# Kernel optimization log

Measured on AMD Instinct MI355X. Metric: run time of the kernel, lower is better.

Reference implementation:

```python
import jax, jax.numpy as jnp
import numpy as np

N, NFEAT, NHID, NCLASS, NLAYERS = 8192, 512, 128, 40, 3
NEG = -9e15

def _sparse_adj(key, n, density=0.002):
    u = jax.random.uniform(key, (n, n), dtype=jnp.float32)
    return jnp.where(u < density, u / density, 0.0)

def setup_inputs() -> dict:
    key = jax.random.key(0)
    ks = jax.random.split(key, 12)
    return {
        "x": jax.random.normal(ks[0], (N, NFEAT), dtype=jnp.float32),
        "adj1": _sparse_adj(ks[1], N),
        "adj2": _sparse_adj(ks[2], N),
        "adj_att": _sparse_adj(ks[3], N),
        "fc1_w": jax.random.normal(ks[4], (NLAYERS, NHID, NFEAT), dtype=jnp.float32) * (1.0 / np.sqrt(NFEAT)),
        "fc1_b": jnp.zeros((NLAYERS, NHID), jnp.float32),
        "Q_w": jax.random.normal(ks[5], (NLAYERS - 1, NHID, NHID), dtype=jnp.float32) * (1.0 / np.sqrt(NHID)),
        "Q_b": jnp.zeros((NLAYERS - 1, NHID), jnp.float32),
        "K_w": jax.random.normal(ks[6], (NLAYERS - 1, NHID, NHID), dtype=jnp.float32) * (1.0 / np.sqrt(NHID)),
        "K_b": jnp.zeros((NLAYERS - 1, NHID), jnp.float32),
        "hop_select": jnp.ones((NLAYERS,), jnp.float32),
        "w": jnp.ones((NLAYERS - 1, 2), jnp.float32),
        "clf_w": jax.random.normal(ks[7], (NCLASS, NHID * NLAYERS), dtype=jnp.float32) * (1.0 / np.sqrt(NHID * NLAYERS)),
        "clf_b": jnp.zeros((NCLASS,), jnp.float32),
    }

def _l2_normalize(x, eps=1e-12):
    # F.normalize(x, p=2, dim=1)
    n = jnp.sqrt(jnp.sum(x * x, axis=1, keepdims=True))
    return x / jnp.maximum(n, eps)

def reference(x, adj1, adj2, adj_att, fc1_w, fc1_b, Q_w, Q_b, K_w, K_b,
              hop_select, w, clf_w, clf_b):
    adj_list = [None, adj1, adj2]
    mask = jax.nn.softmax(hop_select)  # hop selection weights, shape [nlayers]
    outs = []
    for i in range(NLAYERS):
        tmp = x @ fc1_w[i].T + fc1_b[i]  # [N, nhid]
        if adj_list[i] is not None:
            adj = adj_list[i]
            W_att = jax.nn.softmax(w[i - 1])  # [2]
            tmp_att = adj_att @ tmp           # [N, nhid]
            # GCN1: linear then propagate with adj_att (act='None')
            Q = adj_att @ (tmp_att @ Q_w[i - 1].T + Q_b[i - 1])
            K = adj_att @ (tmp_att @ K_w[i - 1].T + K_b[i - 1])
            scores = Q @ K.T                  # [N, N]
            scores = jnp.where(adj > 0, scores, NEG)
            attention = jax.nn.softmax(scores, axis=-1) * W_att[0] + adj * W_att[1]
            tmp = attention @ tmp             # [N, nhid]
        tmp = _l2_normalize(tmp)
        outs.append(mask[i] * tmp)
    final = jnp.concatenate(outs, axis=1)     # [N, nhid*nlayers]
    out = jax.nn.relu(final) @ clf_w.T + clf_b  # dropout is identity in eval
    return jax.nn.log_softmax(out, axis=1)
```

## Files before the change

kernel.cpp:

```cpp
#include <hip/hip_runtime.h>
#include <hip/hip_bf16.h>

#define NN     8192
#define NF4    2048
#define NFEAT  512
#define NHID   128
#define NCLASS 40
#define NLAY   3
#define CAPA   128
#define FSZ    ((size_t)NN * NHID)

typedef float f32x4 __attribute__((ext_vector_type(4)));

__global__ void k_setup(const float* __restrict__ hop, const float* __restrict__ w,
                        float* __restrict__ mask, float* __restrict__ watt,
                        float* __restrict__ colsum) {
    int t = threadIdx.x;
    colsum[t] = 0.f;
    if (t == 0) {
        float m = fmaxf(fmaxf(hop[0], hop[1]), hop[2]);
        float e0 = expf(hop[0] - m), e1 = expf(hop[1] - m), e2 = expf(hop[2] - m);
        float s = e0 + e1 + e2;
        mask[0] = e0 / s; mask[1] = e1 / s; mask[2] = e2 / s;
        for (int l = 0; l < 2; ++l) {
            float a = w[2 * l], b = w[2 * l + 1];
            float mm = fmaxf(a, b);
            float ea = expf(a - mm), eb = expf(b - mm);
            float ss = ea + eb;
            watt[2 * l] = ea / ss; watt[2 * l + 1] = eb / ss;
        }
    }
}

__global__ __launch_bounds__(256) void k_gemm_fc1(
    const float* __restrict__ A, const float* __restrict__ B,
    const float* __restrict__ bias, float* __restrict__ C)
{
    __shared__ float As[32][132];
    __shared__ float Bs[32][132];
    const int tid = threadIdx.x, tx = tid & 15, ty = tid >> 4;
    const int bm = blockIdx.x * 128, bn = blockIdx.y * 128;
    float acc[8][8] = {};

    for (int kt = 0; kt < NFEAT; kt += 32) {
        #pragma unroll
        for (int it = 0; it < 4; ++it) {
            int L = tid + it * 256;
            int r = L >> 3, c4 = (L & 7) * 4;
            f32x4 va = *reinterpret_cast<const f32x4*>(&A[(size_t)(bm + r) * NFEAT + kt + c4]);
            As[c4 + 0][r] = va[0]; As[c4 + 1][r] = va[1]; As[c4 + 2][r] = va[2]; As[c4 + 3][r] = va[3];
            f32x4 vb = *reinterpret_cast<const f32x4*>(&B[(size_t)(bn + r) * NFEAT + kt + c4]);
            Bs[c4 + 0][r] = vb[0]; Bs[c4 + 1][r] = vb[1]; Bs[c4 + 2][r] = vb[2]; Bs[c4 + 3][r] = vb[3];
        }
        __syncthreads();
        #pragma unroll
        for (int kk = 0; kk < 32; ++kk) {
            f32x4 ra0 = *reinterpret_cast<const f32x4*>(&As[kk][ty * 8]);
            f32x4 ra1 = *reinterpret_cast<const f32x4*>(&As[kk][ty * 8 + 4]);
            f32x4 rb0 = *reinterpret_cast<const f32x4*>(&Bs[kk][tx * 8]);
            f32x4 rb1 = *reinterpret_cast<const f32x4*>(&Bs[kk][tx * 8 + 4]);
            float ra[8] = {ra0[0], ra0[1], ra0[2], ra0[3], ra1[0], ra1[1], ra1[2], ra1[3]};
            float rb[8] = {rb0[0], rb0[1], rb0[2], rb0[3], rb1[0], rb1[1], rb1[2], rb1[3]};
            #pragma unroll
            for (int i = 0; i < 8; ++i)
                #pragma unroll
                for (int j = 0; j < 8; ++j)
                    acc[i][j] = fmaf(ra[i], rb[j], acc[i][j]);
        }
        __syncthreads();
    }
    #pragma unroll
    for (int i = 0; i < 8; ++i) {
        int m = bm + ty * 8 + i;
        #pragma unroll
        for (int j = 0; j < 8; ++j) {
            int n = bn + tx * 8 + j;
            C[(size_t)(n >> 7) * FSZ + (size_t)m * NHID + (n & 127)] = acc[i][j] + bias[n];
        }
    }
}

__global__ __launch_bounds__(256) void k_gemm_qkm(
    const float* __restrict__ T2, const float* __restrict__ Qw, const float* __restrict__ Kw,
    const float* __restrict__ Qb, const float* __restrict__ Kb,
    const float* __restrict__ rowsumA, float* __restrict__ QKm)
{
    __shared__ float As[64][68];
    __shared__ float Bs[64][68];
    const int tid = threadIdx.x, tx = tid & 15, ty = tid >> 4;
    const int bm = blockIdx.x * 64, bn = blockIdx.y * 64, Lz = blockIdx.z;
    const float* A = T2 + (size_t)Lz * FSZ;
    const float* Bp; const float* bp; int bc;
    if (bn < 128) { Bp = Qw + (size_t)Lz * NHID * NHID; bp = Qb + (size_t)Lz * NHID; bc = bn; }
    else          { Bp = Kw + (size_t)Lz * NHID * NHID; bp = Kb + (size_t)Lz * NHID; bc = bn - 128; }
    float* C = QKm + (size_t)Lz * NN * 256;
    float acc[4][4] = {};

    for (int kt = 0; kt < NHID; kt += 64) {
        #pragma unroll
        for (int it = 0; it < 4; ++it) {
            int L = tid + it * 256;
            int r = L >> 4, c4 = (L & 15) * 4;
            f32x4 va = *reinterpret_cast<const f32x4*>(&A[(size_t)(bm + r) * NHID + kt + c4]);
            As[c4 + 0][r] = va[0]; As[c4 + 1][r] = va[1]; As[c4 + 2][r] = va[2]; As[c4 + 3][r] = va[3];
            f32x4 vb = *reinterpret_cast<const f32x4*>(&Bp[(size_t)(bc + r) * NHID + kt + c4]);
            Bs[c4 + 0][r] = vb[0]; Bs[c4 + 1][r] = vb[1]; Bs[c4 + 2][r] = vb[2]; Bs[c4 + 3][r] = vb[3];
        }
        __syncthreads();
        #pragma unroll
        for (int kk = 0; kk < 64; ++kk) {
            f32x4 ra4 = *reinterpret_cast<const f32x4*>(&As[kk][ty * 4]);
            f32x4 rb4 = *reinterpret_cast<const f32x4*>(&Bs[kk][tx * 4]);
            #pragma unroll
            for (int i = 0; i < 4; ++i)
                #pragma unroll
                for (int j = 0; j < 4; ++j)
                    acc[i][j] = fmaf(ra4[i], rb4[j], acc[i][j]);
        }
        __syncthreads();
    }
    #pragma unroll
    for (int i = 0; i < 4; ++i) {
        int m = bm + ty * 4 + i;
        float rs = rowsumA[m];
        #pragma unroll
        for (int j = 0; j < 4; ++j) {
            int n = bn + tx * 4 + j;
            C[(size_t)m * 256 + n] = acc[i][j] + rs * bp[bc + tx * 4 + j];
        }
    }
}

__global__ __launch_bounds__(256) void k_extract(
    const float* __restrict__ adj, int* __restrict__ cnt,
    int* __restrict__ cols, float* __restrict__ vals, float* __restrict__ rowsum)
{
    int row = blockIdx.x, t = threadIdx.x;
    __shared__ int lcnt;
    __shared__ float lsum;
    if (t == 0) { lcnt = 0; lsum = 0.f; }
    __syncthreads();
    const f32x4* arow = reinterpret_cast<const f32x4*>(adj + (size_t)row * NN);
    int* rc = cols + (size_t)row * CAPA;
    float* rv = vals + (size_t)row * CAPA;
    for (int c4 = t; c4 < NF4; c4 += 256) {
        f32x4 v = __builtin_nontemporal_load(&arow[c4]);
        #pragma unroll
        for (int k = 0; k < 4; ++k) {
            if (v[k] > 0.f) {
                int p = atomicAdd(&lcnt, 1);
                atomicAdd(&lsum, v[k]);
                if (p < CAPA) { rc[p] = c4 * 4 + k; rv[p] = v[k]; }
            }
        }
    }
    __syncthreads();
    if (t == 0) { cnt[row] = lcnt < CAPA ? lcnt : CAPA; rowsum[row] = lsum; }
}

__global__ __launch_bounds__(256) void k_prep(
    const float* __restrict__ tmps, const float* __restrict__ mask,
    float* __restrict__ outsb, float* __restrict__ colsum)
{
    int b = blockIdx.x, t = threadIdx.x;
    __shared__ float ws[4];
    if (b < NN / 2) {
        int row = b * 2 + (t >> 7), tt = t & 127;
        float v = tmps[(size_t)row * NHID + tt];
        float s = v * v;
        #pragma unroll
        for (int m = 32; m; m >>= 1) s += __shfl_xor(s, m);
        if ((t & 63) == 0) ws[t >> 6] = s;
        __syncthreads();
        int base = (t >> 7) * 2;
        float d = fmaxf(sqrtf(ws[base] + ws[base + 1]), 1e-12f);
        outsb[(size_t)row * (NHID * NLAY) + tt] = mask[0] * v / d;
    } else {
        int b2 = b - NN / 2;
        int L = b2 >> 7, chunk = b2 & 127;
        int col = t & 127, rh = t >> 7;
        const float* X = tmps + (size_t)(L + 1) * FSZ + (size_t)chunk * 64 * NHID;
        float a = 0.f;
        for (int r = rh; r < 64; r += 2) a += X[(size_t)r * NHID + col];
        atomicAdd(&colsum[L * NHID + col], a);
    }
}

__global__ __launch_bounds__(128) void k_spmm128(
    const int* __restrict__ cnt, const int* __restrict__ cols, const float* __restrict__ vals,
    const float* __restrict__ X, float* __restrict__ Y)
{
    int row = blockIdx.x, L = blockIdx.y, t = threadIdx.x;
    const float* Xl = X + (size_t)L * FSZ;
    float* Yl = Y + (size_t)L * FSZ;
    __shared__ int sc[CAPA];
    __shared__ float sv[CAPA];
    int n = cnt[row];
    for (int p = t; p < n; p += 128) { sc[p] = cols[(size_t)row * CAPA + p]; sv[p] = vals[(size_t)row * CAPA + p]; }
    __syncthreads();
    float a0 = 0.f, a1 = 0.f;
    int p = 0;
    for (; p + 2 <= n; p += 2) {
        a0 = fmaf(sv[p],     Xl[(size_t)sc[p]     * NHID + t], a0);
        a1 = fmaf(sv[p + 1], Xl[(size_t)sc[p + 1] * NHID + t], a1);
    }
    if (p < n) a0 = fmaf(sv[p], Xl[(size_t)sc[p] * NHID + t], a0);
    Yl[(size_t)row * NHID + t] = a0 + a1;
}

__global__ __launch_bounds__(256) void k_attn(
    const float* __restrict__ adj1, const float* __restrict__ adj2,
    const float* __restrict__ QKm, const float* __restrict__ tmps,
    const float* __restrict__ colsum, const float* __restrict__ watt,
    const float* __restrict__ mask, float* __restrict__ outsb)
{
    int row = blockIdx.x, L = blockIdx.y, t = threadIdx.x;
    const float* adj = L ? adj2 : adj1;
    const float* QK = QKm + (size_t)L * NN * 256;
    const float* T = tmps + (size_t)(L + 1) * FSZ;
    __shared__ int lcnt;
    __shared__ int cols[CAPA];
    __shared__ float avals[CAPA];
    __shared__ float svals[CAPA];
    __shared__ __align__(16) float qrow[NHID];
    __shared__ float psum[2][NHID];
    __shared__ float ws[4];

    if (t == 0) lcnt = 0;
    if (t < 32) {
        f32x4 q = *reinterpret_cast<const f32x4*>(QK + (size_t)row * 256 + t * 4);
        *reinterpret_cast<f32x4*>(&qrow[t * 4]) = q;
    }
    __syncthreads();

    const f32x4* arow = reinterpret_cast<const f32x4*>(adj + (size_t)row * NN);
    for (int c4 = t; c4 < NF4; c4 += 256) {
        f32x4 v = __builtin_nontemporal_load(&arow[c4]);
        #pragma unroll
        for (int k = 0; k < 4; ++k) {
            if (v[k] > 0.f) {
                int p = atomicAdd(&lcnt, 1);
                if (p < CAPA) { cols[p] = c4 * 4 + k; avals[p] = v[k]; }
            }
        }
    }
    __syncthreads();
    int n = lcnt < CAPA ? lcnt : CAPA;
    float W0 = watt[L * 2], W1 = watt[L * 2 + 1];
    float acc = 0.f;

    if (n > 0) {
        int g = t >> 5, sl = t & 31;
        f32x4 qv = *reinterpret_cast<const f32x4*>(&qrow[sl * 4]);
        for (int p = g; p < n; p += 8) {
            f32x4 kv = *reinterpret_cast<const f32x4*>(QK + (size_t)cols[p] * 256 + 128 + sl * 4);
            float s = qv[0] * kv[0] + qv[1] * kv[1] + qv[2] * kv[2] + qv[3] * kv[3];
            #pragma unroll
            for (int m = 16; m; m >>= 1) s += __shfl_xor(s, m);
            if (sl == 0) svals[p] = s;
        }
        __syncthreads();
        if (t < 64) {
            float mx = -3.0e38f;
            for (int p = t; p < n; p += 64) mx = fmaxf(mx, svals[p]);
            #pragma unroll
            for (int m = 32; m; m >>= 1) mx = fmaxf(mx, __shfl_xor(mx, m));
            float ss = 0.f;
            for (int p = t; p < n; p += 64) ss += expf(svals[p] - mx);
            #pragma unroll
            for (int m = 32; m; m >>= 1) ss += __shfl_xor(ss, m);
            float inv = 1.0f / ss;
            for (int p = t; p < n; p += 64) avals[p] = expf(svals[p] - mx) * inv * W0 + avals[p] * W1;
        }
        __syncthreads();
        int half = t >> 7, tt = t & 127;
        float pacc = 0.f;
        for (int p = half; p < n; p += 2) pacc = fmaf(avals[p], T[(size_t)cols[p] * NHID + tt], pacc);
        psum[half][tt] = pacc;
        __syncthreads();
        if (t < 128) acc = psum[0][t] + psum[1][t];
    } else {
        if (t < 128) acc = W0 * (1.0f / (float)NN) * colsum[L * NHID + t];
    }

    float s2 = acc * acc;
    #pragma unroll
    for (int m = 32; m; m >>= 1) s2 += __shfl_xor(s2, m);
    if ((t & 63) == 0) ws[t >> 6] = s2;
    __syncthreads();
    if (t < 128) {
        float d = fmaxf(sqrtf(ws[0] + ws[1]), 1e-12f);
        outsb[(size_t)row * (NHID * NLAY) + (size_t)(L + 1) * NHID + t] = mask[L + 1] * acc / d;
    }
}

__global__ __launch_bounds__(64) void k_clf(
    const float* __restrict__ outs, const float* __restrict__ Wc,
    const float* __restrict__ bc, float* __restrict__ out)
{
    __shared__ float fin[NHID * NLAY];
    __shared__ float logits[NCLASS];
    int t = threadIdx.x;
    for (int rr = 0; rr < 2; ++rr) {
        int row = blockIdx.x * 2 + rr;
        for (int k = t; k < NHID * NLAY; k += 64) fin[k] = fmaxf(outs[(size_t)row * (NHID * NLAY) + k], 0.f);
        __syncthreads();
        if (t < NCLASS) {
            float acc = bc[t];
            #pragma unroll 4
            for (int k = 0; k < NHID * NLAY; ++k) acc = fmaf(fin[k], Wc[(size_t)t * (NHID * NLAY) + k], acc);
            logits[t] = acc;
        }
        __syncthreads();
        float x = (t < NCLASS) ? logits[t] : -3.0e38f;
        float mx = x;
        #pragma unroll
        for (int m = 32; m; m >>= 1) mx = fmaxf(mx, __shfl_xor(mx, m));
        float e = (t < NCLASS) ? expf(x - mx) : 0.f;
        float ssum = e;
        #pragma unroll
        for (int m = 32; m; m >>= 1) ssum += __shfl_xor(ssum, m);
        if (t < NCLASS) out[(size_t)row * NCLASS + t] = x - mx - logf(ssum);
        __syncthreads();
    }
}

extern "C" void kernel_launch(void* const* d_in, const int* in_sizes, int n_in,
                              void* d_out, int out_size, void* d_ws, size_t ws_size,
                              hipStream_t stream) {
    const float* x       = (const float*)d_in[0];
    const float* adj1    = (const float*)d_in[1];
    const float* adj2    = (const float*)d_in[2];
    const float* adj_att = (const float*)d_in[3];
    const float* fc1_w   = (const float*)d_in[4];
    const float* fc1_b   = (const float*)d_in[5];
    const float* Q_w     = (const float*)d_in[6];
    const float* Q_b     = (const float*)d_in[7];
    const float* K_w     = (const float*)d_in[8];
    const float* K_b     = (const float*)d_in[9];
    const float* hop     = (const float*)d_in[10];
    const float* w       = (const float*)d_in[11];
    const float* clf_w   = (const float*)d_in[12];
    const float* clf_b   = (const float*)d_in[13];

    float* W = (float*)d_ws;
    float* f_mask   = W;
    float* f_watt   = W + 4;
    float* f_colsum = W + 8;
    float* rowsumA  = W + 264;
    float* tmps     = W + 264 + NN;
    float* outsb    = tmps + 3 * FSZ;
    float* tmp_att  = outsb + 3 * FSZ;
    float* T2b      = tmp_att + 2 * FSZ;
    float* QKm      = T2b + 2 * FSZ;
    float* csr_vals = QKm + 4 * FSZ;
    int*   csr_cols = (int*)(csr_vals + FSZ);
    int*   csr_cnt  = csr_cols + FSZ;

    size_t need = (size_t)((char*)(csr_cnt + NN) - (char*)d_ws);
    if (ws_size < need) return;

    k_setup<<<1, 256, 0, stream>>>(hop, w, f_mask, f_watt, f_colsum);

    k_gemm_fc1<<<dim3(NN / 128, (NLAY * NHID) / 128), 256, 0, stream>>>(x, fc1_w, fc1_b, tmps);

    k_extract<<<NN, 256, 0, stream>>>(adj_att, csr_cnt, csr_cols, csr_vals, rowsumA);

    k_prep<<<NN / 2 + 256, 256, 0, stream>>>(tmps, f_mask, outsb, f_colsum);

    k_spmm128<<<dim3(NN, 2), 128, 0, stream>>>(csr_cnt, csr_cols, csr_vals, tmps + FSZ, tmp_att);

    k_spmm128<<<dim3(NN, 2), 128, 0, stream>>>(csr_cnt, csr_cols, csr_vals, tmp_att, T2b);

    k_gemm_qkm<<<dim3(NN / 64, 4, 2), 256, 0, stream>>>(T2b, Q_w, K_w, Q_b, K_b, rowsumA, QKm);

    k_attn<<<dim3(NN, 2), 256, 0, stream>>>(adj1, adj2, QKm, tmps, f_colsum, f_watt, f_mask, outsb);

    k_clf<<<NN / 2, 64, 0, stream>>>(outsb, clf_w, clf_b, (float*)d_out);
}
```

Baseline: 402.2 us.

## Fuse fc1 GEMM with sparse extraction of all three adjacency matrices

Merges the fc1 GEMM, the column-sum reduction and the CSR extraction of adj_att, adj1 and adj2 into one heterogeneous kernel. The attention kernel now reads the precomputed compact lists instead of rescanning the dense adjacency rows, and the l2-normalize of layer 0 is fused with the first SpMM. The aim is to cut launches and let the fc1 compute overlap with the bandwidth-bound adjacency scans. The cost is a larger CSR workspace and a changed fc1 column mapping, which alters the register and LDS access pattern.

```diff
diff --git a/kernel.cpp b/kernel.cpp
--- a/kernel.cpp
+++ b/kernel.cpp
@@ -9,6 +9,7 @@
 #define NLAY   3
 #define CAPA   128
 #define FSZ    ((size_t)NN * NHID)
+#define FC1_GRID 192
 
 typedef float f32x4 __attribute__((ext_vector_type(4)));
 
@@ -32,52 +33,172 @@
     }
 }
 
-__global__ __launch_bounds__(256) void k_gemm_fc1(
-    const float* __restrict__ A, const float* __restrict__ B,
-    const float* __restrict__ bias, float* __restrict__ C)
-{
-    __shared__ float As[32][132];
-    __shared__ float Bs[32][132];
-    const int tid = threadIdx.x, tx = tid & 15, ty = tid >> 4;
-    const int bm = blockIdx.x * 128, bn = blockIdx.y * 128;
-    float acc[8][8] = {};
-
-    for (int kt = 0; kt < NFEAT; kt += 32) {
-        #pragma unroll
-        for (int it = 0; it < 4; ++it) {
-            int L = tid + it * 256;
-            int r = L >> 3, c4 = (L & 7) * 4;
-            f32x4 va = *reinterpret_cast<const f32x4*>(&A[(size_t)(bm + r) * NFEAT + kt + c4]);
-            As[c4 + 0][r] = va[0]; As[c4 + 1][r] = va[1]; As[c4 + 2][r] = va[2]; As[c4 + 3][r] = va[3];
-            f32x4 vb = *reinterpret_cast<const f32x4*>(&B[(size_t)(bn + r) * NFEAT + kt + c4]);
-            Bs[c4 + 0][r] = vb[0]; Bs[c4 + 1][r] = vb[1]; Bs[c4 + 2][r] = vb[2]; Bs[c4 + 3][r] = vb[3];
-        }
-        __syncthreads();
-        #pragma unroll
-        for (int kk = 0; kk < 32; ++kk) {
-            f32x4 ra0 = *reinterpret_cast<const f32x4*>(&As[kk][ty * 8]);
-            f32x4 ra1 = *reinterpret_cast<const f32x4*>(&As[kk][ty * 8 + 4]);
-            f32x4 rb0 = *reinterpret_cast<const f32x4*>(&Bs[kk][tx * 8]);
-            f32x4 rb1 = *reinterpret_cast<const f32x4*>(&Bs[kk][tx * 8 + 4]);
-            float ra[8] = {ra0[0], ra0[1], ra0[2], ra0[3], ra1[0], ra1[1], ra1[2], ra1[3]};
-            float rb[8] = {rb0[0], rb0[1], rb0[2], rb0[3], rb1[0], rb1[1], rb1[2], rb1[3]};
-            #pragma unroll
-            for (int i = 0; i < 8; ++i)
+__global__ __launch_bounds__(256) void k_mega(
+    const float* __restrict__ x, const float* __restrict__ fc1w, const float* __restrict__ fc1b,
+    const float* __restrict__ adjA, const float* __restrict__ adj1, const float* __restrict__ adj2,
+    float* __restrict__ tmps, float* __restrict__ colsum, float* __restrict__ rowsumA,
+    int* __restrict__ cnts, int* __restrict__ colsArr, float* __restrict__ valsArr)
+{
+    __shared__ float smem[8448];
+    __shared__ int s_lcnt;
+    __shared__ float s_lsum;
+    const int b = blockIdx.x, tid = threadIdx.x;
+
+    if (b < FC1_GRID) {
+        float* As = smem;
+        float* Bs = smem + 4224;
+        const int tx = tid & 15, ty = tid >> 4;
+        const int bm = (b & 63) * 128;
+        const int bnt = b >> 6;
+        const int bn = bnt * 128;
+        float acc[8][8] = {};
+
+        for (int kt = 0; kt < NFEAT; kt += 32) {
+            #pragma unroll
+            for (int it = 0; it < 4; ++it) {
+                int L = tid + it * 256;
+                int r = L >> 3, c4 = (L & 7) * 4;
+                f32x4 va = *reinterpret_cast<const f32x4*>(&x[(size_t)(bm + r) * NFEAT + kt + c4]);
+                As[(c4 + 0) * 132 + r] = va[0];
+                As[(c4 + 1) * 132 + r] = va[1];
+                As[(c4 + 2) * 132 + r] = va[2];
+                As[(c4 + 3) * 132 + r] = va[3];
+                f32x4 vb = *reinterpret_cast<const f32x4*>(&fc1w[(size_t)(bn + r) * NFEAT + kt + c4]);
+                Bs[(c4 + 0) * 132 + r] = vb[0];
+                Bs[(c4 + 1) * 132 + r] = vb[1];
+                Bs[(c4 + 2) * 132 + r] = vb[2];
+                Bs[(c4 + 3) * 132 + r] = vb[3];
+            }
+            __syncthreads();
+            #pragma unroll
+            for (int kk = 0; kk < 32; ++kk) {
+                f32x4 ra0 = *reinterpret_cast<const f32x4*>(&As[kk * 132 + ty * 8]);
+                f32x4 ra1 = *reinterpret_cast<const f32x4*>(&As[kk * 132 + ty * 8 + 4]);
+                f32x4 rb0 = *reinterpret_cast<const f32x4*>(&Bs[kk * 132 + tx * 4]);
+                f32x4 rb1 = *reinterpret_cast<const f32x4*>(&Bs[kk * 132 + tx * 4 + 64]);
+                float ra[8] = {ra0[0], ra0[1], ra0[2], ra0[3], ra1[0], ra1[1], ra1[2], ra1[3]};
+                float rb[8] = {rb0[0], rb0[1], rb0[2], rb0[3], rb1[0], rb1[1], rb1[2], rb1[3]};
                 #pragma unroll
-                for (int j = 0; j < 8; ++j)
-                    acc[i][j] = fmaf(ra[i], rb[j], acc[i][j]);
-        }
-        __syncthreads();
-    }
-    #pragma unroll
-    for (int i = 0; i < 8; ++i) {
-        int m = bm + ty * 8 + i;
-        #pragma unroll
-        for (int j = 0; j < 8; ++j) {
-            int n = bn + tx * 8 + j;
-            C[(size_t)(n >> 7) * FSZ + (size_t)m * NHID + (n & 127)] = acc[i][j] + bias[n];
-        }
-    }
+                for (int i = 0; i < 8; ++i)
+                    #pragma unroll
+                    for (int j = 0; j < 8; ++j)
+                        acc[i][j] = fmaf(ra[i], rb[j], acc[i][j]);
+            }
+            __syncthreads();
+        }
+        const float* bofs = fc1b + bn;
+        #pragma unroll
+        for (int i = 0; i < 8; ++i) {
+            int m = bm + ty * 8 + i;
+            #pragma unroll
+            for (int j = 0; j < 8; ++j) {
+                int lc = (j < 4) ? (tx * 4 + j) : (64 + tx * 4 + (j - 4));
+                tmps[(size_t)bnt * FSZ + (size_t)m * NHID + lc] = acc[i][j] + bofs[lc];
+            }
+        }
+        if (bnt >= 1) {
+            #pragma unroll
+            for (int j = 0; j < 8; ++j) {
+                int lc = (j < 4) ? (tx * 4 + j) : (64 + tx * 4 + (j - 4));
+                float s = 8.f * bofs[lc];
+                #pragma unroll
+                for (int i = 0; i < 8; ++i) s += acc[i][j];
+                smem[ty * 128 + lc] = s;
+            }
+            __syncthreads();
+            if (tid < 128) {
+                float s = 0.f;
+                #pragma unroll
+                for (int g = 0; g < 16; ++g) s += smem[g * 128 + tid];
+                atomicAdd(&colsum[(bnt - 1) * NHID + tid], s);
+            }
+        }
+    } else {
+        const int e = b - FC1_GRID;
+        const int mat = e >> 13;
+        const int row = e & (NN - 1);
+        const float* adj = (mat == 0) ? adjA : (mat == 1 ? adj1 : adj2);
+        if (tid == 0) { s_lcnt = 0; s_lsum = 0.f; }
+        __syncthreads();
+        const f32x4* arow = reinterpret_cast<const f32x4*>(adj + (size_t)row * NN);
+        int* rc = colsArr + (size_t)(mat * NN + row) * CAPA;
+        float* rv = valsArr + (size_t)(mat * NN + row) * CAPA;
+        float ls = 0.f;
+        for (int c4 = tid; c4 < NF4; c4 += 256) {
+            f32x4 v = __builtin_nontemporal_load(&arow[c4]);
+            #pragma unroll
+            for (int k = 0; k < 4; ++k) {
+                if (v[k] > 0.f) {
+                    int p = atomicAdd(&s_lcnt, 1);
+                    if (p < CAPA) { rc[p] = c4 * 4 + k; rv[p] = v[k]; }
+                    ls += v[k];
+                }
+            }
+        }
+        if (mat == 0) atomicAdd(&s_lsum, ls);
+        __syncthreads();
+        if (tid == 0) {
+            cnts[mat * NN + row] = s_lcnt < CAPA ? s_lcnt : CAPA;
+            if (mat == 0) rowsumA[row] = s_lsum;
+        }
+    }
+}
+
+__global__ __launch_bounds__(128) void k_sp_norm(
+    const int* __restrict__ cnts, const int* __restrict__ colsArr, const float* __restrict__ valsArr,
+    const float* __restrict__ tmps, const float* __restrict__ mask,
+    float* __restrict__ tmp_att, float* __restrict__ outsb)
+{
+    int row = blockIdx.x, role = blockIdx.y, t = threadIdx.x;
+    __shared__ int sc[CAPA];
+    __shared__ float sv[CAPA];
+    __shared__ float wsn[2];
+    if (role == 2) {
+        float v = tmps[(size_t)row * NHID + t];
+        float s = v * v;
+        #pragma unroll
+        for (int m = 32; m; m >>= 1) s += __shfl_xor(s, m);
+        if ((t & 63) == 0) wsn[t >> 6] = s;
+        __syncthreads();
+        float d = fmaxf(sqrtf(wsn[0] + wsn[1]), 1e-12f);
+        outsb[(size_t)row * (NHID * NLAY) + t] = mask[0] * v / d;
+    } else {
+        const float* X = tmps + (size_t)(role + 1) * FSZ;
+        float* Y = tmp_att + (size_t)role * FSZ;
+        int n = cnts[row];
+        for (int p = t; p < n; p += 128) { sc[p] = colsArr[(size_t)row * CAPA + p]; sv[p] = valsArr[(size_t)row * CAPA + p]; }
+        __syncthreads();
+        float a0 = 0.f, a1 = 0.f;
+        int p = 0;
+        for (; p + 2 <= n; p += 2) {
+            a0 = fmaf(sv[p],     X[(size_t)sc[p]     * NHID + t], a0);
+            a1 = fmaf(sv[p + 1], X[(size_t)sc[p + 1] * NHID + t], a1);
+        }
+        if (p < n) a0 = fmaf(sv[p], X[(size_t)sc[p] * NHID + t], a0);
+        Y[(size_t)row * NHID + t] = a0 + a1;
+    }
+}
+
+__global__ __launch_bounds__(128) void k_spmm2(
+    const int* __restrict__ cnts, const int* __restrict__ colsArr, const float* __restrict__ valsArr,
+    const float* __restrict__ X, float* __restrict__ Y)
+{
+    int row = blockIdx.x, L = blockIdx.y, t = threadIdx.x;
+    const float* Xl = X + (size_t)L * FSZ;
+    float* Yl = Y + (size_t)L * FSZ;
+    __shared__ int sc[CAPA];
+    __shared__ float sv[CAPA];
+    int n = cnts[row];
+    for (int p = t; p < n; p += 128) { sc[p] = colsArr[(size_t)row * CAPA + p]; sv[p] = valsArr[(size_t)row * CAPA + p]; }
+    __syncthreads();
+    float a0 = 0.f, a1 = 0.f;
+    int p = 0;
+    for (; p + 2 <= n; p += 2) {
+        a0 = fmaf(sv[p],     Xl[(size_t)sc[p]     * NHID + t], a0);
+        a1 = fmaf(sv[p + 1], Xl[(size_t)sc[p + 1] * NHID + t], a1);
+    }
+    if (p < n) a0 = fmaf(sv[p], Xl[(size_t)sc[p] * NHID + t], a0);
+    Yl[(size_t)row * NHID + t] = a0 + a1;
 }
 
 __global__ __launch_bounds__(256) void k_gemm_qkm(
@@ -131,94 +252,17 @@
     }
 }
 
-__global__ __launch_bounds__(256) void k_extract(
-    const float* __restrict__ adj, int* __restrict__ cnt,
-    int* __restrict__ cols, float* __restrict__ vals, float* __restrict__ rowsum)
-{
-    int row = blockIdx.x, t = threadIdx.x;
-    __shared__ int lcnt;
-    __shared__ float lsum;
-    if (t == 0) { lcnt = 0; lsum = 0.f; }
-    __syncthreads();
-    const f32x4* arow = reinterpret_cast<const f32x4*>(adj + (size_t)row * NN);
-    int* rc = cols + (size_t)row * CAPA;
-    float* rv = vals + (size_t)row * CAPA;
-    for (int c4 = t; c4 < NF4; c4 += 256) {
-        f32x4 v = __builtin_nontemporal_load(&arow[c4]);
-        #pragma unroll
-        for (int k = 0; k < 4; ++k) {
-            if (v[k] > 0.f) {
-                int p = atomicAdd(&lcnt, 1);
-                atomicAdd(&lsum, v[k]);
-                if (p < CAPA) { rc[p] = c4 * 4 + k; rv[p] = v[k]; }
-            }
-        }
-    }
-    __syncthreads();
-    if (t == 0) { cnt[row] = lcnt < CAPA ? lcnt : CAPA; rowsum[row] = lsum; }
-}
-
-__global__ __launch_bounds__(256) void k_prep(
-    const float* __restrict__ tmps, const float* __restrict__ mask,
-    float* __restrict__ outsb, float* __restrict__ colsum)
-{
-    int b = blockIdx.x, t = threadIdx.x;
-    __shared__ float ws[4];
-    if (b < NN / 2) {
-        int row = b * 2 + (t >> 7), tt = t & 127;
-        float v = tmps[(size_t)row * NHID + tt];
-        float s = v * v;
-        #pragma unroll
-        for (int m = 32; m; m >>= 1) s += __shfl_xor(s, m);
-        if ((t & 63) == 0) ws[t >> 6] = s;
-        __syncthreads();
-        int base = (t >> 7) * 2;
-        float d = fmaxf(sqrtf(ws[base] + ws[base + 1]), 1e-12f);
-        outsb[(size_t)row * (NHID * NLAY) + tt] = mask[0] * v / d;
-    } else {
-        int b2 = b - NN / 2;
-        int L = b2 >> 7, chunk = b2 & 127;
-        int col = t & 127, rh = t >> 7;
-        const float* X = tmps + (size_t)(L + 1) * FSZ + (size_t)chunk * 64 * NHID;
-        float a = 0.f;
-        for (int r = rh; r < 64; r += 2) a += X[(size_t)r * NHID + col];
-        atomicAdd(&colsum[L * NHID + col], a);
-    }
-}
-
-__global__ __launch_bounds__(128) void k_spmm128(
-    const int* __restrict__ cnt, const int* __restrict__ cols, const float* __restrict__ vals,
-    const float* __restrict__ X, float* __restrict__ Y)
-{
-    int row = blockIdx.x, L = blockIdx.y, t = threadIdx.x;
-    const float* Xl = X + (size_t)L * FSZ;
-    float* Yl = Y + (size_t)L * FSZ;
-    __shared__ int sc[CAPA];
-    __shared__ float sv[CAPA];
-    int n = cnt[row];
-    for (int p = t; p < n; p += 128) { sc[p] = cols[(size_t)row * CAPA + p]; sv[p] = vals[(size_t)row * CAPA + p]; }
-    __syncthreads();
-    float a0 = 0.f, a1 = 0.f;
-    int p = 0;
-    for (; p + 2 <= n; p += 2) {
-        a0 = fmaf(sv[p],     Xl[(size_t)sc[p]     * NHID + t], a0);
-        a1 = fmaf(sv[p + 1], Xl[(size_t)sc[p + 1] * NHID + t], a1);
-    }
-    if (p < n) a0 = fmaf(sv[p], Xl[(size_t)sc[p] * NHID + t], a0);
-    Yl[(size_t)row * NHID + t] = a0 + a1;
-}
-
 __global__ __launch_bounds__(256) void k_attn(
-    const float* __restrict__ adj1, const float* __restrict__ adj2,
+    const int* __restrict__ cnts, const int* __restrict__ colsArr, const float* __restrict__ valsArr,
     const float* __restrict__ QKm, const float* __restrict__ tmps,
     const float* __restrict__ colsum, const float* __restrict__ watt,
     const float* __restrict__ mask, float* __restrict__ outsb)
 {
     int row = blockIdx.x, L = blockIdx.y, t = threadIdx.x;
-    const float* adj = L ? adj2 : adj1;
     const float* QK = QKm + (size_t)L * NN * 256;
     const float* T = tmps + (size_t)(L + 1) * FSZ;
-    __shared__ int lcnt;
+    const int* rc = colsArr + (size_t)((1 + L) * NN + row) * CAPA;
+    const float* rv = valsArr + (size_t)((1 + L) * NN + row) * CAPA;
     __shared__ int cols[CAPA];
     __shared__ float avals[CAPA];
     __shared__ float svals[CAPA];
@@ -226,26 +270,12 @@
     __shared__ float psum[2][NHID];
     __shared__ float ws[4];
 
-    if (t == 0) lcnt = 0;
-    if (t < 32) {
-        f32x4 q = *reinterpret_cast<const f32x4*>(QK + (size_t)row * 256 + t * 4);
-        *reinterpret_cast<f32x4*>(&qrow[t * 4]) = q;
-    }
+    int n = cnts[(1 + L) * NN + row];
+    for (int p = t; p < n; p += 256) { cols[p] = rc[p]; avals[p] = rv[p]; }
+    if (t < 32) *reinterpret_cast<f32x4*>(&qrow[t * 4]) =
+        *reinterpret_cast<const f32x4*>(QK + (size_t)row * 256 + t * 4);
     __syncthreads();
 
-    const f32x4* arow = reinterpret_cast<const f32x4*>(adj + (size_t)row * NN);
-    for (int c4 = t; c4 < NF4; c4 += 256) {
-        f32x4 v = __builtin_nontemporal_load(&arow[c4]);
-        #pragma unroll
-        for (int k = 0; k < 4; ++k) {
-            if (v[k] > 0.f) {
-                int p = atomicAdd(&lcnt, 1);
-                if (p < CAPA) { cols[p] = c4 * 4 + k; avals[p] = v[k]; }
-            }
-        }
-    }
-    __syncthreads();
-    int n = lcnt < CAPA ? lcnt : CAPA;
     float W0 = watt[L * 2], W1 = watt[L * 2 + 1];
     float acc = 0.f;
 
@@ -354,27 +384,27 @@
     float* T2b      = tmp_att + 2 * FSZ;
     float* QKm      = T2b + 2 * FSZ;
     float* csr_vals = QKm + 4 * FSZ;
-    int*   csr_cols = (int*)(csr_vals + FSZ);
-    int*   csr_cnt  = csr_cols + FSZ;
-
-    size_t need = (size_t)((char*)(csr_cnt + NN) - (char*)d_ws);
+    int*   csr_cols = (int*)(csr_vals + 3 * FSZ);
+    int*   csr_cnt  = csr_cols + 3 * FSZ;
+
+    size_t need = (size_t)((char*)(csr_cnt + 3 * NN) - (char*)d_ws);
     if (ws_size < need) return;
 
     k_setup<<<1, 256, 0, stream>>>(hop, w, f_mask, f_watt, f_colsum);
 
-    k_gemm_fc1<<<dim3(NN / 128, (NLAY * NHID) / 128), 256, 0, stream>>>(x, fc1_w, fc1_b, tmps);
-
-    k_extract<<<NN, 256, 0, stream>>>(adj_att, csr_cnt, csr_cols, csr_vals, rowsumA);
-
-    k_prep<<<NN / 2 + 256, 256, 0, stream>>>(tmps, f_mask, outsb, f_colsum);
-
-    k_spmm128<<<dim3(NN, 2), 128, 0, stream>>>(csr_cnt, csr_cols, csr_vals, tmps + FSZ, tmp_att);
-
-    k_spmm128<<<dim3(NN, 2), 128, 0, stream>>>(csr_cnt, csr_cols, csr_vals, tmp_att, T2b);
+    k_mega<<<FC1_GRID + 3 * NN, 256, 0, stream>>>(
+        x, fc1_w, fc1_b, adj_att, adj1, adj2,
+        tmps, f_colsum, rowsumA, csr_cnt, csr_cols, csr_vals);
+
+    k_sp_norm<<<dim3(NN, 3), 128, 0, stream>>>(
+        csr_cnt, csr_cols, csr_vals, tmps, f_mask, tmp_att, outsb);
+
+    k_spmm2<<<dim3(NN, 2), 128, 0, stream>>>(csr_cnt, csr_cols, csr_vals, tmp_att, T2b);
 
     k_gemm_qkm<<<dim3(NN / 64, 4, 2), 256, 0, stream>>>(T2b, Q_w, K_w, Q_b, K_b, rowsumA, QKm);
 
-    k_attn<<<dim3(NN, 2), 256, 0, stream>>>(adj1, adj2, QKm, tmps, f_colsum, f_watt, f_mask, outsb);
+    k_attn<<<dim3(NN, 2), 256, 0, stream>>>(
+        csr_cnt, csr_cols, csr_vals, QKm, tmps, f_colsum, f_watt, f_mask, outsb);
 
     k_clf<<<NN / 2, 64, 0, stream>>>(outsb, clf_w, clf_b, (float*)d_out);
 }
```

Measured after the change: 434.0 us. +7.9%, slower.
